# Kernel optimization log

Measured on AMD Instinct MI355X. Metric: run time of the kernel, lower is better.

## Reference

```python
import jax, jax.numpy as jnp
import numpy as np

EMBED = 1024
HEADS = 16
HDIM = EMBED // HEADS
B, S = 4, 2048
NEG = -1e20


def setup_inputs() -> dict:
    key = jax.random.key(0)
    ks = jax.random.split(key, 9)
    query = jax.random.normal(ks[0], (B, S, EMBED), dtype=jnp.float32)
    key_t = jax.random.normal(ks[1], (B, S, EMBED), dtype=jnp.float32)
    value = jax.random.normal(ks[2], (B, S, EMBED), dtype=jnp.float32)
    mask = jax.random.randint(ks[3], (1, 1, S, S), 0, 2, dtype=jnp.int32)
    padding = jax.random.randint(ks[4], (B, 1, 1, S), 0, 2, dtype=jnp.int32)
    sc = 1.0 / np.sqrt(EMBED)
    Wq = jax.random.normal(ks[5], (EMBED, EMBED), dtype=jnp.float32) * sc
    Wk = jax.random.normal(ks[6], (EMBED, EMBED), dtype=jnp.float32) * sc
    Wv = jax.random.normal(ks[7], (EMBED, EMBED), dtype=jnp.float32) * sc
    Wo = jax.random.normal(ks[8], (EMBED, EMBED), dtype=jnp.float32) * sc
    return {"query": query, "key": key_t, "value": value, "mask": mask,
            "padding": padding, "Wq": Wq, "Wk": Wk, "Wv": Wv, "Wo": Wo}


def reference(query, key, value, mask, padding, Wq, Wk, Wv, Wo):
    b, q_len, _ = query.shape
    k_len = key.shape[1]
    # projections (nn.Linear: x @ W^T), split into heads
    qs = (query @ Wq.T).reshape(b, q_len, HEADS, HDIM)
    ks = (key @ Wk.T).reshape(b, k_len, HEADS, HDIM)
    vs = (value @ Wv.T).reshape(b, k_len, HEADS, HDIM)
    scale = EMBED ** 0.25
    qs = qs / scale
    ks = ks / scale
    # [b, h, q, k] scores
    dot = jnp.einsum('bkhd,bqhd->bhqk', ks, qs)
    dot = jnp.where(mask == 0, NEG, dot)
    dot = jnp.where(padding == 0, NEG, dot)
    attn = jax.nn.softmax(dot, axis=-1)
    alpha = jnp.einsum('bhqk,bkhd->bqhd', attn, vs)
    out = alpha.reshape(b, q_len, EMBED) @ Wo.T
    return out
```

## Files before the change

kernel.cpp:

```cpp
#include <hip/hip_runtime.h>
#include <stdint.h>

#define B_  4
#define S_  2048
#define E_  1024
#define H_  16
#define D_  64

typedef __bf16 bf16;
typedef __bf16 bf16x4 __attribute__((ext_vector_type(4)));
typedef __bf16 bf16x8 __attribute__((ext_vector_type(8)));
typedef float  f32x4 __attribute__((ext_vector_type(4)));
typedef float  f32x16 __attribute__((ext_vector_type(16)));
typedef uint32_t u32x4 __attribute__((ext_vector_type(4)));

__device__ __forceinline__ f32x4 mfma16(bf16x8 a, bf16x8 b, f32x4 c) {
  return __builtin_amdgcn_mfma_f32_16x16x32_bf16(a, b, c, 0, 0, 0);
}
__device__ __forceinline__ f32x16 mfma32(bf16x8 a, bf16x8 b, f32x16 c) {
  return __builtin_amdgcn_mfma_f32_32x32x16_bf16(a, b, c, 0, 0, 0);
}

__device__ __forceinline__ int sw(int row, int idx) { return idx ^ ((row & 7) << 3); }

__device__ __forceinline__ void gl_lds16(const void* g, void* l) {
  __builtin_amdgcn_global_load_lds(
      (const __attribute__((address_space(1))) void*)g,
      (__attribute__((address_space(3))) void*)l, 16, 0, 0);
}

__device__ __forceinline__ uint32_t cvtpk(float lo, float hi) {
  uint32_t r;
  asm("v_cvt_pk_bf16_f32 %0, %1, %2" : "=v"(r) : "v"(lo), "v"(hi));
  return r;
}
__device__ __forceinline__ void plswap(uint32_t& a, uint32_t& b) {
  asm("v_permlane32_swap_b32 %0, %1" : "+v"(a), "+v"(b));
}

__global__ void pack_mask_kernel(const int* __restrict__ mask, uint32_t* __restrict__ mbits) {
  int idx = blockIdx.x * 256 + threadIdx.x;
  int q = idx >> 6, w = idx & 63;
  const int* p = mask + q * S_ + w * 32;
  uint32_t bits = 0;
#pragma unroll
  for (int j = 0; j < 32; j += 4) {
    int4 v = *(const int4*)(p + j);
    bits |= (v.x != 0 ? 1u : 0u) << (j + 0);
    bits |= (v.y != 0 ? 1u : 0u) << (j + 1);
    bits |= (v.z != 0 ? 1u : 0u) << (j + 2);
    bits |= (v.w != 0 ? 1u : 0u) << (j + 3);
  }
  mbits[idx] = bits;
}

__global__ void pack_pad_kernel(const int* __restrict__ pad, uint32_t* __restrict__ pbits) {
  int idx = threadIdx.x;
  int b = idx >> 6, w = idx & 63;
  const int* p = pad + b * S_ + w * 32;
  uint32_t bits = 0;
#pragma unroll
  for (int j = 0; j < 32; j += 4) {
    int4 v = *(const int4*)(p + j);
    bits |= (v.x != 0 ? 1u : 0u) << (j + 0);
    bits |= (v.y != 0 ? 1u : 0u) << (j + 1);
    bits |= (v.z != 0 ? 1u : 0u) << (j + 2);
    bits |= (v.w != 0 ? 1u : 0u) << (j + 3);
  }
  pbits[idx] = bits;
}

__global__ __launch_bounds__(256)
void expand_mask(const uint32_t* __restrict__ mbits, const uint32_t* __restrict__ pbits,
                 uint2* __restrict__ mbt) {
  int idx = blockIdx.x * 256 + threadIdx.x;
  int q = idx & 2047;
  int kt = (idx >> 11) & 31;
  int b = idx >> 16;
  uint2 r;
  r.x = mbits[q * 64 + kt * 2 + 0] & pbits[b * 64 + kt * 2 + 0];
  r.y = mbits[q * 64 + kt * 2 + 1] & pbits[b * 64 + kt * 2 + 1];
  mbt[idx] = r;
}

__global__ __launch_bounds__(256)
void cvt_w(const float* __restrict__ w0, const float* __restrict__ w1,
           const float* __restrict__ w2, const float* __restrict__ w3,
           bf16* __restrict__ out, float sq, float sk) {
  int z = blockIdx.z;
  const float* src = z == 0 ? w0 : (z == 1 ? w1 : (z == 2 ? w2 : w3));
  float s = (z == 0) ? sq : ((z == 1) ? sk : 1.0f);
  size_t i = ((size_t)blockIdx.x * 256 + threadIdx.x) * 8;
  float4 a = *(const float4*)(src + i);
  float4 b = *(const float4*)(src + i + 4);
  bf16x8 o;
  o[0] = (bf16)(a.x * s); o[1] = (bf16)(a.y * s); o[2] = (bf16)(a.z * s); o[3] = (bf16)(a.w * s);
  o[4] = (bf16)(b.x * s); o[5] = (bf16)(b.y * s); o[6] = (bf16)(b.z * s); o[7] = (bf16)(b.w * s);
  *(bf16x8*)(out + (size_t)z * (1024ull * 1024ull) + i) = o;
}

struct GA { const void* A; const bf16* W; void* O; };

template<bool A_F32, bool OUT_F32>
__global__ __launch_bounds__(256, 4)
void gemm_bf(GA g0, GA g1, GA g2) {
  GA g = (blockIdx.z == 0) ? g0 : ((blockIdx.z == 1) ? g1 : g2);
  const int id = blockIdx.x;
  const int brow = ((id & 7) * 8 + (id >> 6)) * 128;
  const int bcol = ((id >> 3) & 7) * 128;
  const int tid = threadIdx.x;
  const int l = tid & 63, wv = tid >> 6;
  const int lg = l >> 4, lr = l & 15;
  const int wr = wv >> 1, wc = wv & 1;
  const int sr = l >> 3, sc8 = l & 7;

  __shared__ __align__(16) char smem[32768];
  bf16* As = (bf16*)smem;
  bf16* Bs = (bf16*)(smem + 16384);

  f32x4 acc[4][4] = {};

  const bf16* Bb = g.W + (size_t)(bcol + wv * 32 + sr) * E_ + (size_t)(sc8 ^ sr) * 8;
  bf16* lb = Bs + (wv * 32) * 64;

  const bf16* Abb = nullptr;
  const float* Ap = nullptr;
  f32x4 a0[4], a1[4];
  if constexpr (A_F32) {
    Ap = (const float*)g.A + (size_t)(brow + wv * 32 + sr) * E_ + sc8 * 8;
  } else {
    Abb = (const bf16*)g.A + (size_t)(brow + wv * 32 + sr) * E_ + (size_t)(sc8 ^ sr) * 8;
  }

  auto loadA = [&]() {
#pragma unroll
    for (int i = 0; i < 4; ++i) {
      const float* p = Ap + (size_t)(8 * i) * E_;
      a0[i] = *(const f32x4*)p;
      a1[i] = *(const f32x4*)(p + 4);
    }
    Ap += 64;
  };
  auto writeA = [&]() {
#pragma unroll
    for (int i = 0; i < 4; ++i) {
      int row = wv * 32 + sr + 8 * i;
      u32x4 pk = { cvtpk(a0[i][0], a0[i][1]), cvtpk(a0[i][2], a0[i][3]),
                   cvtpk(a1[i][0], a1[i][1]), cvtpk(a1[i][2], a1[i][3]) };
      *(bf16x8*)&As[sw(row, row * 64 + sc8 * 8)] = __builtin_bit_cast(bf16x8, pk);
    }
  };

  if constexpr (A_F32) loadA();

  for (int kt = 0; kt < E_ / 64; ++kt) {
    __syncthreads();
    if constexpr (A_F32) {
      writeA();
    } else {
      bf16* la = As + (wv * 32) * 64;
      const bf16* a = Abb + kt * 64;
#pragma unroll
      for (int i = 0; i < 4; ++i)
        gl_lds16(a + (size_t)i * 8 * E_, la + i * 8 * 64);
    }
    {
      const bf16* b = Bb + kt * 64;
#pragma unroll
      for (int i = 0; i < 4; ++i)
        gl_lds16(b + (size_t)i * 8 * E_, lb + i * 8 * 64);
    }
    __syncthreads();
    if constexpr (A_F32) {
      if (kt + 1 < E_ / 64) loadA();
    }
#pragma unroll
    for (int kk = 0; kk < 2; ++kk) {
      bf16x8 af[4], bfr[4];
#pragma unroll
      for (int ms = 0; ms < 4; ++ms) {
        int row = wr * 64 + ms * 16 + lr;
        af[ms] = *(const bf16x8*)&As[sw(row, row * 64 + kk * 32 + lg * 8)];
      }
#pragma unroll
      for (int ns = 0; ns < 4; ++ns) {
        int row = wc * 64 + ns * 16 + lr;
        bfr[ns] = *(const bf16x8*)&Bs[sw(row, row * 64 + kk * 32 + lg * 8)];
      }
#pragma unroll
      for (int ms = 0; ms < 4; ++ms)
#pragma unroll
        for (int ns = 0; ns < 4; ++ns)
          acc[ms][ns] = mfma16(af[ms], bfr[ns], acc[ms][ns]);
    }
  }

  if (!OUT_F32 && blockIdx.z == 2) {
    bf16* T = (bf16*)smem;
    __syncthreads();
#pragma unroll
    for (int ms = 0; ms < 4; ++ms) {
#pragma unroll
      for (int ns = 0; ns < 4; ++ns) {
        int col = wc * 64 + ns * 16 + lr;
        int rowb = wr * 64 + ms * 16 + lg * 4;
        bf16x4 hv;
#pragma unroll
        for (int r = 0; r < 4; ++r) hv[r] = (bf16)acc[ms][ns][r];
        *(bf16x4*)&T[col * 128 + (rowb ^ ((col & 7) << 3))] = hv;
      }
    }
    __syncthreads();
    int chunk = tid & 15, dl0 = tid >> 4;
#pragma unroll
    for (int pass = 0; pass < 8; ++pass) {
      int dl = pass * 16 + dl0;
      bf16x8 v = *(const bf16x8*)&T[dl * 128 + ((chunk * 8) ^ ((dl & 7) << 3))];
      int colg = bcol + dl;
      int bh2 = (brow >> 11) * 16 + (colg >> 6);
      int d = colg & 63;
      int s0 = (brow & 2047) + chunk * 8;
      *(bf16x8*)((bf16*)g.O + ((size_t)bh2 * 64 + d) * (size_t)S_ + s0) = v;
    }
    return;
  }

#pragma unroll
  for (int ms = 0; ms < 4; ++ms) {
#pragma unroll
    for (int ns = 0; ns < 4; ++ns) {
#pragma unroll
      for (int r = 0; r < 4; ++r) {
        int row = brow + wr * 64 + ms * 16 + lg * 4 + r;
        int col = bcol + wc * 64 + ns * 16 + lr;
        if constexpr (OUT_F32) ((float*)g.O)[(size_t)row * E_ + col] = acc[ms][ns][r];
        else                   ((bf16*)g.O)[(size_t)row * E_ + col] = (bf16)acc[ms][ns][r];
      }
    }
  }
}

__global__ __launch_bounds__(256, 4)
void attn_kernel(const bf16* __restrict__ Q, const bf16* __restrict__ K,
                 const bf16* __restrict__ Vt, const uint2* __restrict__ mbt,
                 bf16* __restrict__ alpha) {
  const int raw = blockIdx.x;
  const int xcd = raw & 7, slot = raw >> 3;
  const int bh = xcd * 8 + (slot >> 4), qblk = slot & 15;
  const int b = bh >> 4, h = bh & 15;
  const int tid = threadIdx.x, wv = tid >> 6, l = tid & 63;
  const int ln = l & 31, hi = l >> 5;
  const int qw = qblk * 128 + wv * 32;
  const int sr = l >> 3, sc8 = l & 7;
  const int g = (ln & 7) ^ (ln >> 3);

  __shared__ bf16 Ks[2][64 * 64];
  __shared__ bf16 Vs[2][64 * 64];

  bf16x8 qreg[4];
#pragma unroll
  for (int dc = 0; dc < 4; ++dc)
    qreg[dc] = *(const bf16x8*)(Q + (size_t)(b * S_ + qw + ln) * E_ + h * 64 + dc * 16 + hi * 8);

  bf16x8 ones;
#pragma unroll
  for (int j = 0; j < 8; ++j) ones[j] = (bf16)1.0f;

  f32x16 o[2] = {};
  f32x16 lacc = {};

  const int c0 = (sc8 ^ sr ^ ((wv * 2) & 7)) * 8;
  const int c1 = (sc8 ^ sr ^ ((wv * 2 + 1) & 7)) * 8;
  const bf16* kp0 = K + (size_t)(b * S_ + wv * 16 + sr) * E_ + h * 64 + c0;
  const bf16* kp1 = K + (size_t)(b * S_ + wv * 16 + 8 + sr) * E_ + h * 64 + c1;
  const bf16* vp0 = Vt + ((size_t)bh * 64 + wv * 16 + sr) * S_ + c0;
  const bf16* vp1 = Vt + ((size_t)bh * 64 + wv * 16 + 8 + sr) * S_ + c1;
  const uint2* mrow = mbt + ((size_t)b << 16) + qw + ln;

  auto stage = [&](int buf) {
    gl_lds16(kp0, Ks[buf] + (wv * 16) * 64);
    gl_lds16(kp1, Ks[buf] + (wv * 16 + 8) * 64);
    gl_lds16(vp0, Vs[buf] + (wv * 16) * 64);
    gl_lds16(vp1, Vs[buf] + (wv * 16 + 8) * 64);
    kp0 += (size_t)64 * E_;
    kp1 += (size_t)64 * E_;
    vp0 += 64;
    vp1 += 64;
  };

  stage(0);
  __syncthreads();

  for (int kt = 0; kt < 32; ++kt) {
    const int cur = kt & 1;
    if (kt < 31) stage(cur ^ 1);

    f32x16 sc[2] = {};
    __builtin_amdgcn_s_setprio(1);
#pragma unroll
    for (int ct = 0; ct < 2; ++ct) {
#pragma unroll
      for (int dc = 0; dc < 4; ++dc) {
        int row = ct * 32 + ln;
        int c = (dc * 2 + hi) ^ g ^ (ct * 4);
        bf16x8 kf = *(const bf16x8*)&Ks[cur][row * 64 + c * 8];
        sc[ct] = mfma32(kf, qreg[dc], sc[ct]);
      }
    }
    __builtin_amdgcn_s_setprio(0);

    uint2 mv = *mrow;
    mrow += 2048;
    uint32_t mq[2];
    mq[0] = mv.x >> (hi * 4);
    mq[1] = mv.y >> (hi * 4);

    uint32_t up[16];
#pragma unroll
    for (int ct = 0; ct < 2; ++ct) {
      float p[16];
#pragma unroll
      for (int r = 0; r < 16; ++r) {
        const int rel = (r & 3) + 8 * (r >> 2);
        float pe = __builtin_amdgcn_exp2f(sc[ct][r]);
        uint32_t keep = (uint32_t)__builtin_amdgcn_sbfe(mq[ct], rel, 1);
        p[r] = __builtin_bit_cast(float, __builtin_bit_cast(uint32_t, pe) & keep);
      }
#pragma unroll
      for (int j = 0; j < 8; ++j)
        up[ct * 8 + j] = cvtpk(p[2 * j], p[2 * j + 1]);
    }

#pragma unroll
    for (int kc = 0; kc < 4; ++kc) {
      const int ct = kc >> 1, base = ct * 8 + (kc & 1) * 4;
      plswap(up[base + 0], up[base + 2]);
      plswap(up[base + 1], up[base + 3]);
      u32x4 w = {up[base + 0], up[base + 1], up[base + 2], up[base + 3]};
      bf16x8 pf = __builtin_bit_cast(bf16x8, w);
      __builtin_amdgcn_s_setprio(1);
#pragma unroll
      for (int dt = 0; dt < 2; ++dt) {
        int row = dt * 32 + ln;
        int c = (kc * 2 + hi) ^ g ^ (dt * 4);
        bf16x8 vf = *(const bf16x8*)&Vs[cur][row * 64 + c * 8];
        o[dt] = mfma32(vf, pf, o[dt]);
      }
      lacc = mfma32(ones, pf, lacc);
      __builtin_amdgcn_s_setprio(0);
    }
    __syncthreads();
  }

  float inv = 1.0f / lacc[0];
  size_t qoff = (size_t)(b * S_ + qw + ln) * E_ + h * 64;
#pragma unroll
  for (int dt = 0; dt < 2; ++dt) {
#pragma unroll
    for (int rg = 0; rg < 4; ++rg) {
      bf16x4 ov;
#pragma unroll
      for (int j = 0; j < 4; ++j) ov[j] = (bf16)(o[dt][rg * 4 + j] * inv);
      *(bf16x4*)(alpha + qoff + dt * 32 + rg * 8 + hi * 4) = ov;
    }
  }
}

extern "C" void kernel_launch(void* const* d_in, const int* in_sizes, int n_in,
                              void* d_out, int out_size, void* d_ws, size_t ws_size,
                              hipStream_t stream) {
  const float* query = (const float*)d_in[0];
  const float* key_t = (const float*)d_in[1];
  const float* value = (const float*)d_in[2];
  const int*   mask  = (const int*)d_in[3];
  const int*   pad   = (const int*)d_in[4];
  const float* Wq    = (const float*)d_in[5];
  const float* Wk    = (const float*)d_in[6];
  const float* Wv    = (const float*)d_in[7];
  const float* Wo    = (const float*)d_in[8];

  char* ws = (char*)d_ws;
  bf16* alpha = (bf16*)ws;
  bf16* Wb    = (bf16*)(ws + ((size_t)16 << 20));
  bf16* QKV   = (bf16*)(ws + ((size_t)24 << 20));
  uint32_t* mbits = (uint32_t*)(ws + ((size_t)72 << 20));
  uint32_t* pbits = mbits + (size_t)S_ * 64;
  uint2*    mbt   = (uint2*)(ws + ((size_t)73 << 20));

  const size_t AM = 8192ull * 1024ull;
  const size_t WM = 1024ull * 1024ull;
  bf16* Vt = QKV + 2 * AM;

  pack_mask_kernel<<<512, 256, 0, stream>>>(mask, mbits);
  pack_pad_kernel<<<1, 256, 0, stream>>>(pad, pbits);
  expand_mask<<<1024, 256, 0, stream>>>(mbits, pbits, mbt);

  const float qscale = 0.17677669529663687f;
  const float log2e  = 1.4426950408889634f;
  cvt_w<<<dim3(512, 1, 4), 256, 0, stream>>>(Wq, Wk, Wv, Wo, Wb, qscale * log2e, qscale);

  GA gq{query, Wb,          QKV};
  GA gk{key_t, Wb + WM,     QKV + AM};
  GA gv{value, Wb + 2 * WM, Vt};
  gemm_bf<true, false><<<dim3(512, 1, 3), 256, 0, stream>>>(gq, gk, gv);

  attn_kernel<<<1024, 256, 0, stream>>>(QKV, QKV + AM, Vt, mbt, alpha);

  GA go{alpha, Wb + 3 * WM, d_out};
  gemm_bf<false, true><<<dim3(512, 1, 1), 256, 0, stream>>>(go, go, go);
}
```

Before: 210.1 us.

## Double-buffer GEMM B tiles and triple-buffer attention K/V with manual waitcnt

The GEMM now double-buffers the weight (B) tile in shared memory and prefetches the next tile before the compute barrier, waiting only on older loads via explicit vmcnt. The attention kernel moves to a three-stage K/V ring buffer with two tiles in flight, prefetches the mask word one iteration ahead, and drops the trailing __syncthreads in favour of a single waitcnt+barrier per iteration. This hides global-to-LDS latency behind MFMA work at the cost of more shared memory, so occupancy bounds drop from 4 to 3 blocks per CU. The hand-written vmcnt counts must match the number of outstanding loads exactly, or the pipeline becomes a race.

```diff
diff --git a/kernel.cpp b/kernel.cpp
--- a/kernel.cpp
+++ b/kernel.cpp
@@ -102,7 +102,7 @@
 struct GA { const void* A; const bf16* W; void* O; };
 
 template<bool A_F32, bool OUT_F32>
-__global__ __launch_bounds__(256, 4)
+__global__ __launch_bounds__(256, 3)
 void gemm_bf(GA g0, GA g1, GA g2) {
   GA g = (blockIdx.z == 0) ? g0 : ((blockIdx.z == 1) ? g1 : g2);
   const int id = blockIdx.x;
@@ -113,15 +113,22 @@
   const int lg = l >> 4, lr = l & 15;
   const int wr = wv >> 1, wc = wv & 1;
   const int sr = l >> 3, sc8 = l & 7;
-
-  __shared__ __align__(16) char smem[32768];
+  const int NT = E_ / 64;
+
+  __shared__ __align__(16) char smem[49152];
   bf16* As = (bf16*)smem;
-  bf16* Bs = (bf16*)(smem + 16384);
+  bf16* BsB = (bf16*)(smem + 16384);
 
   f32x4 acc[4][4] = {};
 
   const bf16* Bb = g.W + (size_t)(bcol + wv * 32 + sr) * E_ + (size_t)(sc8 ^ sr) * 8;
-  bf16* lb = Bs + (wv * 32) * 64;
+  auto stageB = [&](int buf) {
+    bf16* lb = BsB + buf * (128 * 64) + (wv * 32) * 64;
+#pragma unroll
+    for (int i = 0; i < 4; ++i)
+      gl_lds16(Bb + (size_t)i * 8 * E_, lb + i * 8 * 64);
+    Bb += 64;
+  };
 
   const bf16* Abb = nullptr;
   const float* Ap = nullptr;
@@ -151,10 +158,11 @@
     }
   };
 
+  stageB(0);
   if constexpr (A_F32) loadA();
 
-  for (int kt = 0; kt < E_ / 64; ++kt) {
-    __syncthreads();
+  for (int kt = 0; kt < NT; ++kt) {
+    __builtin_amdgcn_s_barrier();
     if constexpr (A_F32) {
       writeA();
     } else {
@@ -164,16 +172,17 @@
       for (int i = 0; i < 4; ++i)
         gl_lds16(a + (size_t)i * 8 * E_, la + i * 8 * 64);
     }
-    {
-      const bf16* b = Bb + kt * 64;
-#pragma unroll
-      for (int i = 0; i < 4; ++i)
-        gl_lds16(b + (size_t)i * 8 * E_, lb + i * 8 * 64);
-    }
-    __syncthreads();
+    if (kt + 1 < NT) {
+      stageB(kt + 1 < NT ? ((kt + 1) & 1) : 0);
+      asm volatile("s_waitcnt vmcnt(4) lgkmcnt(0)" ::: "memory");
+    } else {
+      asm volatile("s_waitcnt vmcnt(0) lgkmcnt(0)" ::: "memory");
+    }
+    __builtin_amdgcn_s_barrier();
     if constexpr (A_F32) {
-      if (kt + 1 < E_ / 64) loadA();
-    }
+      if (kt + 1 < NT) loadA();
+    }
+    const bf16* bsc = BsB + (kt & 1) * (128 * 64);
 #pragma unroll
     for (int kk = 0; kk < 2; ++kk) {
       bf16x8 af[4], bfr[4];
@@ -185,7 +194,7 @@
 #pragma unroll
       for (int ns = 0; ns < 4; ++ns) {
         int row = wc * 64 + ns * 16 + lr;
-        bfr[ns] = *(const bf16x8*)&Bs[sw(row, row * 64 + kk * 32 + lg * 8)];
+        bfr[ns] = *(const bf16x8*)&bsc[sw(row, row * 64 + kk * 32 + lg * 8)];
       }
 #pragma unroll
       for (int ms = 0; ms < 4; ++ms)
@@ -240,7 +249,7 @@
   }
 }
 
-__global__ __launch_bounds__(256, 4)
+__global__ __launch_bounds__(256, 3)
 void attn_kernel(const bf16* __restrict__ Q, const bf16* __restrict__ K,
                  const bf16* __restrict__ Vt, const uint2* __restrict__ mbt,
                  bf16* __restrict__ alpha) {
@@ -254,8 +263,8 @@
   const int sr = l >> 3, sc8 = l & 7;
   const int g = (ln & 7) ^ (ln >> 3);
 
-  __shared__ bf16 Ks[2][64 * 64];
-  __shared__ bf16 Vs[2][64 * 64];
+  __shared__ bf16 Ks[3][64 * 64];
+  __shared__ bf16 Vs[3][64 * 64];
 
   bf16x8 qreg[4];
 #pragma unroll
@@ -288,12 +297,19 @@
     vp1 += 64;
   };
 
+  uint2 mv = *mrow;
+  mrow += 2048;
   stage(0);
-  __syncthreads();
-
+  stage(1);
+
+  int cur = 0, sbuf = 2;
   for (int kt = 0; kt < 32; ++kt) {
-    const int cur = kt & 1;
-    if (kt < 31) stage(cur ^ 1);
+    asm volatile("s_waitcnt vmcnt(4)" ::: "memory");
+    __builtin_amdgcn_s_barrier();
+
+    uint2 mv_nxt = *mrow;
+    mrow += 2048;
+    stage(sbuf);
 
     f32x16 sc[2] = {};
     __builtin_amdgcn_s_setprio(1);
@@ -309,8 +325,6 @@
     }
     __builtin_amdgcn_s_setprio(0);
 
-    uint2 mv = *mrow;
-    mrow += 2048;
     uint32_t mq[2];
     mq[0] = mv.x >> (hi * 4);
     mq[1] = mv.y >> (hi * 4);
@@ -349,7 +363,10 @@
       lacc = mfma32(ones, pf, lacc);
       __builtin_amdgcn_s_setprio(0);
     }
-    __syncthreads();
+
+    mv = mv_nxt;
+    cur = (cur == 2) ? 0 : cur + 1;
+    sbuf = (sbuf == 2) ? 0 : sbuf + 1;
   }
 
   float inv = 1.0f / lacc[0];
```

Result: slower. 215.2 us (+2.4%).
